# Kernel tuning notes

Measured on AMD Instinct MI355X. Metric: run time of the kernel, lower is better.

Reference implementation:

```python
import jax, jax.numpy as jnp
import numpy as np

NUM_LABELS = 1000


def setup_inputs() -> dict:
    key = jax.random.key(0)
    k1, k2 = jax.random.split(key)
    outputs = jax.random.normal(k1, (64, 512, NUM_LABELS), dtype=jnp.float32)
    labels = jax.random.randint(k2, (64, 512), 0, NUM_LABELS, dtype=jnp.int32)
    return {"outputs": outputs, "labels": labels}


def reference(outputs, labels):
    L = outputs.shape[-1]
    flat = outputs.reshape(-1, L)        # [N, L]
    labs = labels.reshape(-1)            # [N]

    # State: index_selection [L] (the permutation torch derives via
    # argmax(encode_transfer, 1)) and unswitched-label membership mask [L].
    # torch.inner(ET, eye[select_col]) permutes ET's COLUMNS by select_col
    # (a transposition), which composes onto index_selection as
    # new_idx = select_col[old_idx].
    def step(carry, xs):
        idx_sel, unsw = carry
        y, lab = xs
        r = jnp.argmax(y[idx_sel]).astype(idx_sel.dtype)  # switched argmax
        lab_unsw = unsw[lab]
        do_swap = (r != lab) & lab_unsw
        # apply transposition (r <-> lab) to idx_sel when do_swap
        swapped = jnp.where(idx_sel == r, lab,
                            jnp.where(idx_sel == lab, r, idx_sel))
        new_idx = jnp.where(do_swap, swapped, idx_sel)
        # label is removed from unswitched set whenever it was a member
        # (both the mismatch-swap branch and the match branch remove it)
        new_unsw = unsw.at[lab].set(False)
        return (new_idx, new_unsw), None

    init = (jnp.arange(L, dtype=jnp.int32), jnp.ones((L,), dtype=bool))
    (idx_final, _), _ = jax.lax.scan(step, init, (flat, labs))

    # torch returns index_select on the flattened outputs with the FINAL
    # index_selection
    return jnp.take(flat, idx_final, axis=-1)
```

## Files before the change

### kernel.cpp

```cpp
#include <hip/hip_runtime.h>
#include <climits>
#include <cstdint>

#define L 1000
#define NROWS 32768


__global__ void k_init(int* __restrict__ first_row, int* __restrict__ evt_slot) {
    int i = blockIdx.x * blockDim.x + threadIdx.x;
    if (i < NROWS) evt_slot[i] = -1;
    if (i < L) first_row[i] = INT_MAX;
}

__global__ void k_first(const int* __restrict__ labels, int* __restrict__ first_row) {
    int i = blockIdx.x * blockDim.x + threadIdx.x;
    if (i < NROWS) atomicMin(&first_row[labels[i]], i);
}

__global__ void k_argmax(const float* __restrict__ flat, const int* __restrict__ first_row,
                         int* __restrict__ evt_slot) {
    int lab = blockIdx.x;
    int row = first_row[lab];
    if (row == INT_MAX) return;
    const float* y = flat + (size_t)row * L;
    int tid = threadIdx.x;
    float bv = -INFINITY;
    int bk = 0x7fffffff;
    for (int k = tid; k < L; k += 256) {
        float v = y[k];
        if (v > bv) { bv = v; bk = k; }
    }
    __shared__ float sv[256];
    __shared__ int   sk[256];
    sv[tid] = bv; sk[tid] = bk;
    __syncthreads();
    for (int off = 128; off > 0; off >>= 1) {
        if (tid < off) {
            float v2 = sv[tid + off]; int k2 = sk[tid + off];
            if (v2 > sv[tid] || (v2 == sv[tid] && k2 < sk[tid])) { sv[tid] = v2; sk[tid] = k2; }
        }
        __syncthreads();
    }
    if (tid == 0) evt_slot[row] = (lab << 10) | sk[0];
}

__global__ void __launch_bounds__(1024) k_seq(const int* __restrict__ evt_slot,
                                              int* __restrict__ perm_g) {
    __shared__ int evt[L];
    __shared__ int pos[L];
    __shared__ int scnt[1024];
    int tid = threadIdx.x;
    int base = tid * 32;
    int c = 0;
    for (int j = 0; j < 32; j++) c += (evt_slot[base + j] >= 0) ? 1 : 0;
    scnt[tid] = c;
    __syncthreads();
    for (int off = 1; off < 1024; off <<= 1) {
        int v = scnt[tid];
        int add = (tid >= off) ? scnt[tid - off] : 0;
        __syncthreads();
        scnt[tid] = v + add;
        __syncthreads();
    }
    int K = scnt[1023];
    int w = tid ? scnt[tid - 1] : 0;
    for (int j = 0; j < 32; j++) {
        int v = evt_slot[base + j];
        if (v >= 0) evt[w++] = v;
    }
    if (tid < L) pos[tid] = tid;
    __syncthreads();
    if (tid == 0) {
        for (int i = 0; i < K; i++) {
            int v = evt[i];
            int lab = v >> 10;
            int m = v & 1023;
            int r = pos[m];
            if (r != lab) {
                int pr = pos[r];
                int pl = pos[lab];
                pos[r] = pl;
                pos[lab] = pr;
            }
        }
    }
    __syncthreads();
    if (tid < L) perm_g[pos[tid]] = tid;
}

#define RPB 8
__global__ void k_gather(const float* __restrict__ flat, const int* __restrict__ perm_g,
                         float* __restrict__ out) {
    __shared__ __align__(16) int   p[L];
    __shared__ __align__(16) float buf[L];
    int tid = threadIdx.x;
    for (int j = tid; j < L; j += 256) p[j] = perm_g[j];
    int row0 = blockIdx.x * RPB;
    for (int rr = 0; rr < RPB; rr++) {
        size_t off = (size_t)(row0 + rr) * L;
        __syncthreads();
        if (tid < 250) ((float4*)buf)[tid] = ((const float4*)(flat + off))[tid];
        __syncthreads();
        if (tid < 250) {
            int j = tid * 4;
            float4 o;
            o.x = buf[p[j + 0]];
            o.y = buf[p[j + 1]];
            o.z = buf[p[j + 2]];
            o.w = buf[p[j + 3]];
            ((float4*)(out + off))[tid] = o;
        }
    }
}

extern "C" void kernel_launch(void* const* d_in, const int* in_sizes, int n_in,
                              void* d_out, int out_size, void* d_ws, size_t ws_size,
                              hipStream_t stream) {
    const float* flat   = (const float*)d_in[0];
    const int*   labels = (const int*)d_in[1];
    float* out = (float*)d_out;
    int* ws = (int*)d_ws;
    int* first_row = ws;
    int* perm_g    = ws + 1024;
    int* evt_slot  = ws + 2048;

    k_init  <<<(NROWS + 255) / 256, 256, 0, stream>>>(first_row, evt_slot);
    k_first <<<(NROWS + 255) / 256, 256, 0, stream>>>(labels, first_row);
    k_argmax<<<L, 256, 0, stream>>>(flat, first_row, evt_slot);
    k_seq   <<<1, 1024, 0, stream>>>(evt_slot, perm_g);
    k_gather<<<NROWS / RPB, 256, 0, stream>>>(flat, perm_g, out);
}
```

Measured before the change: 372.7 us.

## Software-pipeline serial swap loop and restructure gather to four rows per block

The single-thread sequential swap loop now prefetches the next event's label and position lookups before the current swap and patches them when the swap touches the same entries, which shortens the dependent shared-memory latency chain. The gather kernel now uses 1024-thread blocks with four row groups, each loading one row into registers before the permutation barrier, instead of looping over eight rows with two barriers per row. The aim is more memory parallelism per block and fewer serial barriers. The forwarding logic in the serial loop adds correctness risk.

Result: faster. 351.1 us (-5.8%).

```diff
diff --git a/kernel.cpp b/kernel.cpp
--- a/kernel.cpp
+++ b/kernel.cpp
@@ -46,7 +46,7 @@
 
 __global__ void __launch_bounds__(1024) k_seq(const int* __restrict__ evt_slot,
                                               int* __restrict__ perm_g) {
-    __shared__ int evt[L];
+    __shared__ int evt[1025];
     __shared__ int pos[L];
     __shared__ int scnt[1024];
     int tid = threadIdx.x;
@@ -70,46 +70,58 @@
     }
     if (tid < L) pos[tid] = tid;
     __syncthreads();
-    if (tid == 0) {
+    if (tid == 0 && K > 0) {
+        evt[K] = evt[K - 1];
+        int v0 = evt[0];
+        int lab = v0 >> 10, m = v0 & 1023;
+        int Pm = pos[m], Plab = pos[lab];
         for (int i = 0; i < K; i++) {
-            int v = evt[i];
-            int lab = v >> 10;
-            int m = v & 1023;
-            int r = pos[m];
+            int vn   = evt[i + 1];
+            int labn = vn >> 10, mn = vn & 1023;
+            int Pmn   = pos[mn];
+            int Plabn = pos[labn];
+            int r = Pm;
             if (r != lab) {
                 int pr = pos[r];
-                int pl = pos[lab];
-                pos[r] = pl;
+                pos[r]   = Plab;
                 pos[lab] = pr;
+                if (mn == r)        Pmn = Plab;
+                else if (mn == lab) Pmn = pr;
+                if (labn == r)        Plabn = Plab;
+                else if (labn == lab) Plabn = pr;
             }
+            Pm = Pmn; Plab = Plabn; lab = labn; m = mn;
         }
     }
     __syncthreads();
     if (tid < L) perm_g[pos[tid]] = tid;
 }
 
-#define RPB 8
-__global__ void k_gather(const float* __restrict__ flat, const int* __restrict__ perm_g,
-                         float* __restrict__ out) {
-    __shared__ __align__(16) int   p[L];
-    __shared__ __align__(16) float buf[L];
+__global__ void __launch_bounds__(1024) k_gather(const float* __restrict__ flat,
+                                                 const int* __restrict__ perm_g,
+                                                 float* __restrict__ out) {
+    __shared__ __align__(16) int   p[1024];
+    __shared__ __align__(16) float buf[4][L];
     int tid = threadIdx.x;
-    for (int j = tid; j < L; j += 256) p[j] = perm_g[j];
-    int row0 = blockIdx.x * RPB;
-    for (int rr = 0; rr < RPB; rr++) {
-        size_t off = (size_t)(row0 + rr) * L;
-        __syncthreads();
-        if (tid < 250) ((float4*)buf)[tid] = ((const float4*)(flat + off))[tid];
-        __syncthreads();
-        if (tid < 250) {
-            int j = tid * 4;
-            float4 o;
-            o.x = buf[p[j + 0]];
-            o.y = buf[p[j + 1]];
-            o.z = buf[p[j + 2]];
-            o.w = buf[p[j + 3]];
-            ((float4*)(out + off))[tid] = o;
-        }
+    if (tid < L) p[tid] = perm_g[tid];
+    int g = tid >> 8;
+    int t = tid & 255;
+    size_t row = (size_t)blockIdx.x * 4 + g;
+    const float* src = flat + row * L;
+    float*       dst = out  + row * L;
+    float4 v;
+    if (t < 250) v = ((const float4*)src)[t];
+    __syncthreads();
+    if (t < 250) ((float4*)buf[g])[t] = v;
+    __syncthreads();
+    if (t < 250) {
+        int j = t * 4;
+        float4 o;
+        o.x = buf[g][p[j + 0]];
+        o.y = buf[g][p[j + 1]];
+        o.z = buf[g][p[j + 2]];
+        o.w = buf[g][p[j + 3]];
+        ((float4*)dst)[t] = o;
     }
 }
 
@@ -128,5 +140,5 @@
     k_first <<<(NROWS + 255) / 256, 256, 0, stream>>>(labels, first_row);
     k_argmax<<<L, 256, 0, stream>>>(flat, first_row, evt_slot);
     k_seq   <<<1, 1024, 0, stream>>>(evt_slot, perm_g);
-    k_gather<<<NROWS / RPB, 256, 0, stream>>>(flat, perm_g, out);
+    k_gather<<<NROWS / 4, 1024, 0, stream>>>(flat, perm_g, out);
 }
```
